# Kernel tuning notes

Hardware: AMD Instinct MI355X
Metric: run time of the kernel (lower is better)

Reference implementation:

```python
import jax, jax.numpy as jnp
import numpy as np

B, N_PER, DEG, F_IN, F_HID = 64, 1024, 16, 128, 128
E = B * N_PER * DEG  # 1,048,576 edges, grouped per graph


def setup_inputs() -> dict:
    key = jax.random.key(0)
    ks = jax.random.split(key, 16)
    n_total = B * N_PER
    x = jax.random.normal(ks[0], (n_total, F_IN), dtype=jnp.float32)
    # edges are random within each graph block
    local = jax.random.randint(ks[1], (2, E), 0, N_PER)
    offs = (jnp.arange(E, dtype=jnp.int64) // (N_PER * DEG)) * N_PER
    edge_index = (local.astype(jnp.int64) + offs[None, :])
    edge_weight = jax.random.uniform(ks[2], (E,), dtype=jnp.float32)
    batch_index = jnp.repeat(jnp.arange(B, dtype=jnp.int64), N_PER)
    s = 1.0 / np.sqrt(F_HID)
    params = {
        'W1': jax.random.normal(ks[3], (F_IN, F_HID)) * s,
        'b1': jnp.zeros((F_HID,), jnp.float32),
        'p1': jax.random.normal(ks[4], (F_HID,)) * s,
        'W2': jax.random.normal(ks[5], (F_HID, F_HID)) * s,
        'b2': jnp.zeros((F_HID,), jnp.float32),
        'p2': jax.random.normal(ks[6], (F_HID,)) * s,
        'W3': jax.random.normal(ks[7], (F_HID, F_HID)) * s,
        'b3': jnp.zeros((F_HID,), jnp.float32),
        'p3': jax.random.normal(ks[8], (F_HID,)) * s,
        'Wo': jax.random.normal(ks[9], (2 * F_HID, 1)) * s,
        'bo': jnp.zeros((1,), jnp.float32),
    }
    return {'x': x, 'edge_index': edge_index, 'edge_weight': edge_weight,
            'batch_index': batch_index, **params}


def _gcn_conv(x, src, dst, w, W, b):
    # GCNConv with add_self_loops=True, symmetric normalization, edge_weight.
    n = x.shape[0]
    xW = x @ W
    deg = jnp.zeros((n,), x.dtype).at[dst].add(w) + 1.0  # +1 from self-loop fill
    dinv = jax.lax.rsqrt(deg)
    norm = dinv[src] * w * dinv[dst]
    agg = jnp.zeros_like(xW).at[dst].add(norm[:, None] * xW[src])
    return agg + (dinv * dinv)[:, None] * xW + b  # self-loop term + bias


def _topk_pool(x, src, dst, w, p, n, k):
    # TopKPooling with nonlinearity=sigmoid, equal-size graphs (n -> k nodes).
    f = x.shape[1]
    xr = x.reshape(B, n, f)
    score = jax.nn.sigmoid((xr @ p) / jnp.linalg.norm(p))  # [B, n]
    vals, perm = jax.lax.top_k(score, k)                    # per-graph top-k
    xn = jnp.take_along_axis(xr, perm[:, :, None], axis=1) * vals[:, :, None]
    # inverse map old local idx -> new local idx (-1 if dropped)
    inv = jnp.full((B, n), -1, dtype=jnp.int32)
    inv = inv.at[jnp.arange(B)[:, None], perm].set(jnp.arange(k, dtype=jnp.int32)[None, :])
    g = src // n
    sl = inv[g, src % n]
    dl = inv[dst // n, dst % n]
    keep = (sl >= 0) & (dl >= 0)
    # dropped edges are masked to node 0 with weight 0 (contribute nothing)
    src2 = jnp.where(keep, g * k + sl, 0)
    dst2 = jnp.where(keep, (dst // n) * k + dl, 0)
    w2 = jnp.where(keep, w, jnp.zeros((), w.dtype))
    return xn.reshape(B * k, f), src2, dst2, w2


def reference(x, edge_index, edge_weight, batch_index,
              W1, b1, p1, W2, b2, p2, W3, b3, p3, Wo, bo):
    src, dst = edge_index[0], edge_index[1]
    w = edge_weight
    n = N_PER
    h = _gcn_conv(x, src, dst, w, W1, b1)
    h, src, dst, w = _topk_pool(h, src, dst, w, p1, n, n // 2); n //= 2
    h = jax.nn.relu(h)
    h = _gcn_conv(h, src, dst, w, W2, b2)
    h, src, dst, w = _topk_pool(h, src, dst, w, p2, n, n // 2); n //= 2
    h = jax.nn.relu(h)
    h = _gcn_conv(h, src, dst, w, W3, b3)
    h, src, dst, w = _topk_pool(h, src, dst, w, p3, n, n // 2); n //= 2
    h = jax.nn.relu(h)
    hr = h.reshape(B, n, -1)
    cat = jnp.concatenate([hr.max(axis=1), hr.mean(axis=1)], axis=1)  # gmp || gap
    out = jax.nn.sigmoid(cat @ Wo + bo)
    return out, cat
```

## Files before the change

kernel.cpp:

```cpp
#include <hip/hip_runtime.h>

#define NB 64
#define EDGES 1048576
#define NTOT  65536

struct __align__(8) CsrE { int s; float w; };

using bf16x8 = __attribute__((ext_vector_type(8))) short;
using f32x4  = __attribute__((ext_vector_type(4))) float;

__global__ void k_zerof(float* __restrict__ p, int n){
  int i=blockIdx.x*256+threadIdx.x; if(i<n) p[i]=0.f;
}

__device__ inline void split1(float x, unsigned &hi16, unsigned &lo16){
  unsigned b=__float_as_uint(x);
  unsigned h=(b+0x7FFFu+((b>>16)&1u))&0xFFFF0000u;
  float lf=x-__uint_as_float(h);
  unsigned lb=__float_as_uint(lf);
  hi16=h>>16;
  lo16=(lb+0x7FFFu+((lb>>16)&1u))>>16;
}

__device__ inline void split8(const float4&u, const float4&v, bf16x8&hi, bf16x8&lo){
  float e[8]={u.x,u.y,u.z,u.w,v.x,v.y,v.z,v.w};
  #pragma unroll
  for(int j=0;j<8;++j){
    unsigned h16,l16; split1(e[j],h16,l16);
    hi[j]=(short)h16; lo[j]=(short)l16;
  }
}

__global__ __launch_bounds__(256) void k_cntpack(const int* __restrict__ edst,
        const float* __restrict__ ew, int* __restrict__ chunkcnt, float* __restrict__ chunkw,
        const float* __restrict__ W1, const float* __restrict__ W2,
        const float* __restrict__ W3, unsigned* __restrict__ outp){
  __shared__ int lc[1024];
  __shared__ float lw[1024];
  int b=blockIdx.x, tid=threadIdx.x;
  if(b<512){
    int xcd=b&7, slot=b>>3;
    int graph=xcd*8+(slot&7), chunk=slot>>3;
    int e0=graph*16384+chunk*2048;
    for(int t=tid;t<1024;t+=256){ lc[t]=0; lw[t]=0.f; }
    __syncthreads();
    for(int e=e0+tid; e<e0+2048; e+=256){
      int dl=edst[e]&1023;
      atomicAdd(&lc[dl],1);
      atomicAdd(&lw[dl],ew[e]);
    }
    __syncthreads();
    for(int t=tid;t<1024;t+=256){
      chunkcnt[chunk*65536+graph*1024+t]=lc[t];
      chunkw  [chunk*65536+graph*1024+t]=lw[t];
    }
  } else {
    int wb=b-512, m=wb>>3;
    const float* W = (m==0)?W1:((m==1)?W2:W3);
    unsigned* o = outp + m*16384;
    for(int t=(wb&7)*256+tid; t<8192; t+=2048){
      int i=t&3, l=(t>>2)&63, c=(t>>8)&7, q=(t>>11)&3;
      int col=c*16+(l&15);
      int k0=q*32+((l>>4)<<3)+i*2;
      float x0=W[k0*128+col], x1=W[(k0+1)*128+col];
      unsigned h0,l0,h1,l1;
      split1(x0,h0,l0); split1(x1,h1,l1);
      int base=((q*8+c)*2)*256;
      o[base + l*4 + i]       = (h1<<16)|h0;
      o[base + 256 + l*4 + i] = (l1<<16)|l0;
    }
  }
}

template<bool G, int S>
__global__ __launch_bounds__(256) void mm_mfma(const float* __restrict__ X,
        const unsigned* __restrict__ Wpk, const int* __restrict__ selold,
        const float* __restrict__ score, float* __restrict__ Y, int gshift){
  __shared__ __align__(16) unsigned Wl[16384];
  const int RPB = 64*S;
  int b=blockIdx.x;
  int row0b;
  if(G){
    int xcd=b&7, slot=b>>3, bpg=1<<gshift;
    int graph=xcd*8+(slot>>gshift), idx=slot&(bpg-1);
    row0b = graph*(bpg*RPB) + idx*RPB;
  } else row0b = b*RPB;
  for(int t=threadIdx.x;t<4096;t+=256)
    ((uint4*)Wl)[t]=((const uint4*)Wpk)[t];
  const int wave=threadIdx.x>>6, lane=threadIdx.x&63;
  const int row0 = row0b + wave*(16*S);
  const int lrow=lane&15, lko=(lane>>4)<<3;
  int orow[S]; float scr[S];
  #pragma unroll
  for(int s=0;s<S;++s){
    int rr=row0+s*16+lrow;
    orow[s]=G?selold[rr]:rr;
    scr[s]=G?score[orow[s]]:1.f;
  }
  const f32x4 vzero={0.f,0.f,0.f,0.f};
  f32x4 acc[S][8];
  #pragma unroll
  for(int s=0;s<S;++s){
    #pragma unroll
    for(int c=0;c<8;++c) acc[s][c]=vzero;
  }
  __syncthreads();
  const char* wb=(const char*)Wl + lane*16;
  float4 u[S],v[S];
  #pragma unroll
  for(int s=0;s<S;++s){
    const float* xp=X+(size_t)orow[s]*128+lko;
    u[s]=*(const float4*)xp; v[s]=*(const float4*)(xp+4);
  }
  #pragma unroll
  for(int q=0;q<4;++q){
    float4 un[S],vn[S];
    if(q<3){
      #pragma unroll
      for(int s=0;s<S;++s){
        const float* xp=X+(size_t)orow[s]*128+(q+1)*32+lko;
        un[s]=*(const float4*)xp; vn[s]=*(const float4*)(xp+4);
      }
    }
    bf16x8 Ah[S],Al[S];
    #pragma unroll
    for(int s=0;s<S;++s){
      if(G){
        u[s].x=fmaxf(u[s].x*scr[s],0.f); u[s].y=fmaxf(u[s].y*scr[s],0.f);
        u[s].z=fmaxf(u[s].z*scr[s],0.f); u[s].w=fmaxf(u[s].w*scr[s],0.f);
        v[s].x=fmaxf(v[s].x*scr[s],0.f); v[s].y=fmaxf(v[s].y*scr[s],0.f);
        v[s].z=fmaxf(v[s].z*scr[s],0.f); v[s].w=fmaxf(v[s].w*scr[s],0.f);
      }
      split8(u[s],v[s],Ah[s],Al[s]);
    }
    #pragma unroll
    for(int c=0;c<8;++c){
      const bf16x8 bh=*(const bf16x8*)(wb + (q*8+c)*2048);
      const bf16x8 bl=*(const bf16x8*)(wb + (q*8+c)*2048 + 1024);
      #pragma unroll
      for(int s=0;s<S;++s){
        acc[s][c]=__builtin_amdgcn_mfma_f32_16x16x32_bf16(Ah[s],bh,acc[s][c],0,0,0);
        acc[s][c]=__builtin_amdgcn_mfma_f32_16x16x32_bf16(Al[s],bh,acc[s][c],0,0,0);
        acc[s][c]=__builtin_amdgcn_mfma_f32_16x16x32_bf16(Ah[s],bl,acc[s][c],0,0,0);
      }
    }
    if(q<3){
      #pragma unroll
      for(int s=0;s<S;++s){ u[s]=un[s]; v[s]=vn[s]; }
    }
  }
  const int dcol=lane&15, dr0=(lane>>4)<<2;
  #pragma unroll
  for(int s=0;s<S;++s){
    #pragma unroll
    for(int c=0;c<8;++c){
      #pragma unroll
      for(int r=0;r<4;++r){
        Y[(size_t)(row0+s*16+dr0+r)*128 + c*16 + dcol]=acc[s][c][r];
      }
    }
  }
}

__global__ __launch_bounds__(1024) void k_scatter2(const int* __restrict__ esrc,
        const int* __restrict__ edst, const float* __restrict__ ew,
        const int* __restrict__ chunkcnt, const float* __restrict__ chunkw,
        int* __restrict__ rowptr, float* __restrict__ dinv1, CsrE* __restrict__ csr){
  __shared__ int lc[1024];
  __shared__ int wsum[16];
  int b=blockIdx.x, i=threadIdx.x;
  int lane=i&63, w=i>>6;
  int xcd=b&7, slot=b>>3;
  int graph=xcd*8+(slot&7), chunk=slot>>3;
  int o=graph*1024+i;
  int ck[8];
  int c=0;
  #pragma unroll
  for(int k=0;k<8;++k){ ck[k]=chunkcnt[k*65536+o]; c+=ck[k]; }
  int v=c;
  #pragma unroll
  for(int off=1;off<64;off<<=1){ int t=__shfl_up(v,off,64); if(lane>=off) v+=t; }
  if(lane==63) wsum[w]=v;
  __syncthreads();
  int base=0;
  for(int k=0;k<w;++k) base+=wsum[k];
  int excl=base+v-c;
  int r0=graph*16384+excl;
  if(chunk==0){
    rowptr[o]=r0;
    float ws=0.f;
    #pragma unroll
    for(int k=0;k<8;++k) ws+=chunkw[k*65536+o];
    dinv1[o]=rsqrtf(ws+1.0f);
    if(graph==63 && i==1023) rowptr[65536]=EDGES;
  }
  int myfill=r0;
  for(int k=0;k<chunk;++k) myfill+=ck[k];
  lc[i]=myfill;
  __syncthreads();
  int e0=graph*16384+chunk*2048;
  for(int e=e0+i; e<e0+2048; e+=1024){
    int dl=edst[e]&1023;
    int pos=atomicAdd(&lc[dl],1);
    CsrE ce; ce.s=esrc[e]; ce.w=ew[e];
    csr[pos]=ce;
  }
}

template<bool F>
__global__ __launch_bounds__(256) void k_gather(const float* __restrict__ xw, const CsrE* __restrict__ csr,
        const int* __restrict__ rowptr, const int* __restrict__ map, const int* __restrict__ inv,
        const float* __restrict__ dinvv, const float* __restrict__ bias, const float* __restrict__ p,
        float* __restrict__ h, float* __restrict__ score, int gshift, int ns){
  int wv=threadIdx.x>>6, half=(threadIdx.x>>5)&1, hl=threadIdx.x&31;
  int b=blockIdx.x, xcd=b&7, slot=b>>3, bpg=1<<gshift;
  int graph=xcd*8+(slot>>gshift), idx=slot&(bpg-1);
  int v = graph*(bpg<<3) + (idx<<3) + wv*2 + half;
  if(v>=ns) return;
  int d0 = F? map[v] : v;
  float dv=dinvv[v];
  int rs=rowptr[d0], re=rowptr[d0+1];
  const int f4=hl*4;
  float4 accA={0.f,0.f,0.f,0.f}, accB={0.f,0.f,0.f,0.f};
  for(int base=rs; base<re; base+=32){
    int len=re-base; if(len>32) len=32;
    int sidx=0; float cf=0.f;
    if(hl<len){
      CsrE en=csr[base+hl];
      int s=en.s; bool live=true;
      if(F){ int t=inv[s]; live=(t>=0); s=live?t:0; }
      if(live){ sidx=s; cf=dinvv[s]*en.w; }
    }
    int len4=(len+3)&~3;
    for(int j=0;j<len4;j+=4){
      float c0=__shfl(cf,j,32),   c1=__shfl(cf,j+1,32);
      float c2=__shfl(cf,j+2,32), c3=__shfl(cf,j+3,32);
      int   s0=__shfl(sidx,j,32),   s1=__shfl(sidx,j+1,32);
      int   s2=__shfl(sidx,j+2,32), s3=__shfl(sidx,j+3,32);
      const float4 x0=*(const float4*)&xw[(size_t)s0*128+f4];
      const float4 x1=*(const float4*)&xw[(size_t)s1*128+f4];
      const float4 x2=*(const float4*)&xw[(size_t)s2*128+f4];
      const float4 x3=*(const float4*)&xw[(size_t)s3*128+f4];
      accA.x+=c0*x0.x; accA.y+=c0*x0.y; accA.z+=c0*x0.z; accA.w+=c0*x0.w;
      accB.x+=c1*x1.x; accB.y+=c1*x1.y; accB.z+=c1*x1.z; accB.w+=c1*x1.w;
      accA.x+=c2*x2.x; accA.y+=c2*x2.y; accA.z+=c2*x2.z; accA.w+=c2*x2.w;
      accB.x+=c3*x3.x; accB.y+=c3*x3.y; accB.z+=c3*x3.z; accB.w+=c3*x3.w;
    }
  }
  float4 acc; acc.x=accA.x+accB.x; acc.y=accA.y+accB.y;
  acc.z=accA.z+accB.z; acc.w=accA.w+accB.w;
  const float4 xv=*(const float4*)&xw[(size_t)v*128+f4];
  const float4 bv=*(const float4*)&bias[f4];
  float d2=dv*dv;
  float4 hv;
  hv.x=acc.x*dv + d2*xv.x + bv.x;
  hv.y=acc.y*dv + d2*xv.y + bv.y;
  hv.z=acc.z*dv + d2*xv.z + bv.z;
  hv.w=acc.w*dv + d2*xv.w + bv.w;
  *(float4*)&h[(size_t)v*128+f4]=hv;
  const float4 pv=*(const float4*)&p[f4];
  float z=hv.x*pv.x+hv.y*pv.y+hv.z*pv.z+hv.w*pv.w;
  float pp=pv.x*pv.x+pv.y*pv.y+pv.z*pv.z+pv.w*pv.w;
  #pragma unroll
  for(int m=16;m>0;m>>=1){ z+=__shfl_xor(z,m,32); pp+=__shfl_xor(pp,m,32); }
  if(hl==0) score[v]=1.0f/(1.0f+expf(-z/sqrtf(pp)));
}

template<int N, int K, int MODE>
__global__ __launch_bounds__(N) void k_topk(const float* __restrict__ score,
        int* __restrict__ inv, int* __restrict__ selold,
        const int* __restrict__ inv1s, const int* __restrict__ sel1s,
        int* __restrict__ inv12, int* __restrict__ map12,
        const int* __restrict__ rowptr, const CsrE* __restrict__ csr,
        float* __restrict__ dinv_out,
        const float* __restrict__ h3, const float* __restrict__ Wo,
        const float* __restrict__ bo, float* __restrict__ outp){
  __shared__ unsigned hist[256];
  __shared__ int wsum[16];
  __shared__ int c_sh, r_sh;
  __shared__ float red[128];
  int g=blockIdx.x, i=threadIdx.x;
  int lane=i&63, w=i>>6;
  int gv=g*N+i;
  unsigned key=__float_as_uint(score[gv]);
  int st=1;
  int R=K;
  #pragma unroll
  for(int pass=0; pass<4; ++pass){
    int shift=24-pass*8;
    if(i<256) hist[i]=0;
    __syncthreads();
    unsigned byte=(key>>shift)&255u;
    if(st==1) atomicAdd(&hist[byte],1u);
    __syncthreads();
    unsigned hcnt=0, sfx=0;
    if(i<256){
      hcnt=hist[i]; sfx=hcnt;
      #pragma unroll
      for(int off=1;off<64;off<<=1){
        unsigned t=__shfl_down(sfx,off,64);
        if(lane+off<64) sfx+=t;
      }
      if(lane==0) wsum[w]=(int)sfx;
    }
    __syncthreads();
    if(i<256){
      int tot=0;
      for(int k=w+1;k<4;++k) tot+=wsum[k];
      int Si=(int)sfx+tot;
      int A=Si-(int)hcnt;
      if(A<R && R<=Si){ c_sh=i; r_sh=R-A; }
    }
    __syncthreads();
    int c=c_sh; R=r_sh;
    if(st==1){
      if((int)byte>c) st=2;
      else if((int)byte<c) st=0;
    }
    __syncthreads();
  }
  int alive=(st==1)?1:0;
  unsigned long long mA=__ballot(alive);
  int rA=__popcll(mA & ((1ULL<<lane)-1ULL));
  if(lane==0) wsum[w]=__popcll(mA);
  __syncthreads();
  int offA=0;
  for(int k=0;k<w;++k) offA+=wsum[k];
  int tie_rank=offA+rA;
  int sel=(st==2)||(st==1 && tie_rank<R);
  __syncthreads();
  unsigned long long mS=__ballot(sel);
  int rS=__popcll(mS & ((1ULL<<lane)-1ULL));
  if(lane==0) wsum[w]=__popcll(mS);
  __syncthreads();
  int offS=0;
  for(int k=0;k<w;++k) offS+=wsum[k];
  int ng=g*K+offS+rS;
  if(sel && ng<NB*K){ inv[gv]=ng; selold[ng]=gv; }
  else inv[gv]=-1;
  if(MODE==1){
    __syncthreads();
    for(int t=i; t<K; t+=N){
      int v=g*K+t;
      int d0=selold[v];
      int rs=rowptr[d0], re=rowptr[d0+1];
      float s0=0.f,s1=0.f,s2=0.f,s3=0.f;
      int e=rs;
      for(; e+4<=re; e+=4){
        CsrE e0=csr[e], e1=csr[e+1], e2=csr[e+2], e3=csr[e+3];
        if(inv[e0.s]>=0) s0+=e0.w;
        if(inv[e1.s]>=0) s1+=e1.w;
        if(inv[e2.s]>=0) s2+=e2.w;
        if(inv[e3.s]>=0) s3+=e3.w;
      }
      for(; e<re; ++e){
        CsrE en=csr[e];
        if(inv[en.s]>=0) s0+=en.w;
      }
      dinv_out[v]=rsqrtf((s0+s1)+(s2+s3)+1.0f);
    }
  }
  if(MODE==2){
    __syncthreads();
    for(int t=i; t<1024; t+=N){
      int v0=g*1024+t;
      int q=inv1s[v0];
      inv12[v0]=(q>=0)?inv[q]:-1;
    }
    for(int t=i; t<K; t+=N){
      int v=g*K+t;
      map12[v]=sel1s[selold[v]];
    }
    __syncthreads();
    for(int t=i; t<K; t+=N){
      int v=g*K+t;
      int d0=map12[v];
      int rs=rowptr[d0], re=rowptr[d0+1];
      float s0=0.f,s1=0.f,s2=0.f,s3=0.f;
      int e=rs;
      for(; e+4<=re; e+=4){
        CsrE e0=csr[e], e1=csr[e+1], e2=csr[e+2], e3=csr[e+3];
        if(inv12[e0.s]>=0) s0+=e0.w;
        if(inv12[e1.s]>=0) s1+=e1.w;
        if(inv12[e2.s]>=0) s2+=e2.w;
        if(inv12[e3.s]>=0) s3+=e3.w;
      }
      for(; e<re; ++e){
        CsrE en=csr[e];
        if(inv12[en.s]>=0) s0+=en.w;
      }
      dinv_out[v]=rsqrtf((s0+s1)+(s2+s3)+1.0f);
    }
  }
  if(MODE==3){
    __syncthreads();
    int f=i;
    float mx=-3.4e38f, sm=0.f;
    if(f<128){
      for(int nd=0;nd<128;++nd){
        int old=selold[g*128+nd];
        float vv=fmaxf(h3[(size_t)old*128+f]*score[old],0.f);
        mx=fmaxf(mx,vv); sm+=vv;
      }
      float mean=sm*(1.0f/128.0f);
      outp[64+g*256+f]    =mx;
      outp[64+g*256+128+f]=mean;
      red[f]=mx*Wo[f]+mean*Wo[128+f];
    }
    __syncthreads();
    for(int off=64;off>0;off>>=1){
      if(f<off) red[f]+=red[f+off];
      __syncthreads();
    }
    if(f==0){ float z=red[0]+bo[0]; outp[g]=1.0f/(1.0f+expf(-z)); }
  }
}

extern "C" void kernel_launch(void* const* d_in, const int* in_sizes, int n_in,
                              void* d_out, int out_size, void* d_ws, size_t ws_size,
                              hipStream_t stream) {
  (void)in_sizes; (void)n_in;
  const float* x  = (const float*)d_in[0];
  const int*   ei = (const int*)d_in[1];
  const float* ew = (const float*)d_in[2];
  const float* W1=(const float*)d_in[4];  const float* b1=(const float*)d_in[5];  const float* p1=(const float*)d_in[6];
  const float* W2=(const float*)d_in[7];  const float* b2=(const float*)d_in[8];  const float* p2=(const float*)d_in[9];
  const float* W3=(const float*)d_in[10]; const float* b3=(const float*)d_in[11]; const float* p3=(const float*)d_in[12];
  const float* Wo=(const float*)d_in[13]; const float* bo=(const float*)d_in[14];
  float* out=(float*)d_out;

  char* ws=(char*)d_ws;
  size_t cur=0;
  float* slot0=(float*)(ws+cur); cur+=33554432;
  float* slot1=(float*)(ws+cur); cur+=33554432;
  CsrE*  csr  =(CsrE*)(ws+cur);  cur+=(size_t)EDGES*8;
  int*   chunkcnt=(int*)(ws+cur); cur+=2097152;
  float* chunkw  =(float*)(ws+cur); cur+=2097152;
  int*   rowptr=(int*) (ws+cur); cur+=262400;
  float* dinv1=(float*)(ws+cur); cur+=262144;
  float* dinv2=(float*)(ws+cur); cur+=131072;
  float* dinv3=(float*)(ws+cur); cur+=65536;
  float* sc1  =(float*)(ws+cur); cur+=262144;
  float* sc2  =(float*)(ws+cur); cur+=131072;
  float* sc3  =(float*)(ws+cur); cur+=65536;
  int*   inv1 =(int*)  (ws+cur); cur+=262144;
  int*   inv2 =(int*)  (ws+cur); cur+=131072;
  int*   invS =(int*)  (ws+cur); cur+=65536;
  int*   inv12=(int*)  (ws+cur); cur+=262144;
  int*   sel1 =(int*)  (ws+cur); cur+=131072;
  int*   sel2 =(int*)  (ws+cur); cur+=65536;
  int*   sel3 =(int*)  (ws+cur); cur+=32768;
  int*   map12=(int*)  (ws+cur); cur+=65536;
  unsigned* wpk=(unsigned*)(ws+cur); cur+=196608;

  if (ws_size < cur) {
    k_zerof<<<(out_size+255)/256,256,0,stream>>>(out,out_size);
    return;
  }

  const int* esrc=ei; const int* edst=ei+EDGES;

  k_cntpack<<<536,256,0,stream>>>(edst,ew,chunkcnt,chunkw,W1,W2,W3,wpk);
  mm_mfma<false,2><<<NTOT/128,256,0,stream>>>(x,wpk,nullptr,nullptr,slot0,0);
  k_scatter2<<<512,1024,0,stream>>>(esrc,edst,ew,chunkcnt,chunkw,rowptr,dinv1,csr);
  k_gather<false><<<NTOT/8,256,0,stream>>>(slot0,csr,rowptr,nullptr,nullptr,
                                           dinv1,b1,p1,slot1,sc1,7,NTOT);
  k_topk<1024,512,1><<<NB,1024,0,stream>>>(sc1,inv1,sel1,nullptr,nullptr,nullptr,nullptr,
                                           rowptr,csr,dinv2,nullptr,nullptr,nullptr,nullptr);

  mm_mfma<true,1><<<32768/64,256,0,stream>>>(slot1,wpk+16384,sel1,sc1,slot0,3);
  k_gather<true><<<32768/8,256,0,stream>>>(slot0,csr,rowptr,sel1,inv1,
                                           dinv2,b2,p2,slot1,sc2,6,32768);
  k_topk<512,256,2><<<NB,512,0,stream>>>(sc2,inv2,sel2,inv1,sel1,inv12,map12,
                                         rowptr,csr,dinv3,nullptr,nullptr,nullptr,nullptr);

  mm_mfma<true,1><<<16384/64,256,0,stream>>>(slot1,wpk+32768,sel2,sc2,slot0,2);
  k_gather<true><<<16384/8,256,0,stream>>>(slot0,csr,rowptr,map12,inv12,
                                           dinv3,b3,p3,slot1,sc3,5,16384);
  k_topk<256,128,3><<<NB,256,0,stream>>>(sc3,invS,sel3,nullptr,nullptr,nullptr,nullptr,
                                         nullptr,nullptr,nullptr,slot1,Wo,bo,out);
}
```

Before: 270.4 us.

## Move post-topk degree recomputation into extra blocks of the following matmul kernel

The pooled-graph degree/dinv computation (and the inv12/map12 remapping) previously ran inside the top-k kernel, using only 64 blocks with long serial per-thread loops. It now runs as extra blocks appended to the next mm_mfma launch, so it is spread across more blocks and overlaps with the matmul work. The risk is load imbalance among the mixed blocks. A mode-3 block also depends on inv12 values written by other threads of the same block, which relies on the __syncthreads placement within that block being correct.

```diff
diff --git a/kernel.cpp b/kernel.cpp
--- a/kernel.cpp
+++ b/kernel.cpp
@@ -72,93 +72,147 @@
   }
 }
 
-template<bool G, int S>
+template<bool G, int S, int EPI, int MMB>
 __global__ __launch_bounds__(256) void mm_mfma(const float* __restrict__ X,
         const unsigned* __restrict__ Wpk, const int* __restrict__ selold,
-        const float* __restrict__ score, float* __restrict__ Y, int gshift){
+        const float* __restrict__ score, float* __restrict__ Y, int gshift,
+        const int* __restrict__ inv1, const int* __restrict__ sel1,
+        const int* __restrict__ inv2, const int* __restrict__ sel2,
+        int* __restrict__ inv12, int* __restrict__ map12,
+        const int* __restrict__ rowptr, const CsrE* __restrict__ csr,
+        float* __restrict__ dinv_out){
   __shared__ __align__(16) unsigned Wl[16384];
-  const int RPB = 64*S;
   int b=blockIdx.x;
-  int row0b;
-  if(G){
-    int xcd=b&7, slot=b>>3, bpg=1<<gshift;
-    int graph=xcd*8+(slot>>gshift), idx=slot&(bpg-1);
-    row0b = graph*(bpg*RPB) + idx*RPB;
-  } else row0b = b*RPB;
-  for(int t=threadIdx.x;t<4096;t+=256)
-    ((uint4*)Wl)[t]=((const uint4*)Wpk)[t];
-  const int wave=threadIdx.x>>6, lane=threadIdx.x&63;
-  const int row0 = row0b + wave*(16*S);
-  const int lrow=lane&15, lko=(lane>>4)<<3;
-  int orow[S]; float scr[S];
-  #pragma unroll
-  for(int s=0;s<S;++s){
-    int rr=row0+s*16+lrow;
-    orow[s]=G?selold[rr]:rr;
-    scr[s]=G?score[orow[s]]:1.f;
-  }
-  const f32x4 vzero={0.f,0.f,0.f,0.f};
-  f32x4 acc[S][8];
-  #pragma unroll
-  for(int s=0;s<S;++s){
-    #pragma unroll
-    for(int c=0;c<8;++c) acc[s][c]=vzero;
-  }
-  __syncthreads();
-  const char* wb=(const char*)Wl + lane*16;
-  float4 u[S],v[S];
-  #pragma unroll
-  for(int s=0;s<S;++s){
-    const float* xp=X+(size_t)orow[s]*128+lko;
-    u[s]=*(const float4*)xp; v[s]=*(const float4*)(xp+4);
-  }
-  #pragma unroll
-  for(int q=0;q<4;++q){
-    float4 un[S],vn[S];
-    if(q<3){
+  if(b<MMB){
+    const int RPB = 64*S;
+    int row0b;
+    if(G){
+      int xcd=b&7, slot=b>>3, bpg=1<<gshift;
+      int graph=xcd*8+(slot>>gshift), idx=slot&(bpg-1);
+      row0b = graph*(bpg*RPB) + idx*RPB;
+    } else row0b = b*RPB;
+    for(int t=threadIdx.x;t<4096;t+=256)
+      ((uint4*)Wl)[t]=((const uint4*)Wpk)[t];
+    const int wave=threadIdx.x>>6, lane=threadIdx.x&63;
+    const int row0 = row0b + wave*(16*S);
+    const int lrow=lane&15, lko=(lane>>4)<<3;
+    int orow[S]; float scr[S];
+    #pragma unroll
+    for(int s=0;s<S;++s){
+      int rr=row0+s*16+lrow;
+      orow[s]=G?selold[rr]:rr;
+      scr[s]=G?score[orow[s]]:1.f;
+    }
+    const f32x4 vzero={0.f,0.f,0.f,0.f};
+    f32x4 acc[S][8];
+    #pragma unroll
+    for(int s=0;s<S;++s){
+      #pragma unroll
+      for(int c=0;c<8;++c) acc[s][c]=vzero;
+    }
+    __syncthreads();
+    const char* wb=(const char*)Wl + lane*16;
+    float4 u[S],v[S];
+    #pragma unroll
+    for(int s=0;s<S;++s){
+      const float* xp=X+(size_t)orow[s]*128+lko;
+      u[s]=*(const float4*)xp; v[s]=*(const float4*)(xp+4);
+    }
+    #pragma unroll
+    for(int q=0;q<4;++q){
+      float4 un[S],vn[S];
+      if(q<3){
+        #pragma unroll
+        for(int s=0;s<S;++s){
+          const float* xp=X+(size_t)orow[s]*128+(q+1)*32+lko;
+          un[s]=*(const float4*)xp; vn[s]=*(const float4*)(xp+4);
+        }
+      }
+      bf16x8 Ah[S],Al[S];
       #pragma unroll
       for(int s=0;s<S;++s){
-        const float* xp=X+(size_t)orow[s]*128+(q+1)*32+lko;
-        un[s]=*(const float4*)xp; vn[s]=*(const float4*)(xp+4);
-      }
-    }
-    bf16x8 Ah[S],Al[S];
+        if(G){
+          u[s].x=fmaxf(u[s].x*scr[s],0.f); u[s].y=fmaxf(u[s].y*scr[s],0.f);
+          u[s].z=fmaxf(u[s].z*scr[s],0.f); u[s].w=fmaxf(u[s].w*scr[s],0.f);
+          v[s].x=fmaxf(v[s].x*scr[s],0.f); v[s].y=fmaxf(v[s].y*scr[s],0.f);
+          v[s].z=fmaxf(v[s].z*scr[s],0.f); v[s].w=fmaxf(v[s].w*scr[s],0.f);
+        }
+        split8(u[s],v[s],Ah[s],Al[s]);
+      }
+      #pragma unroll
+      for(int c=0;c<8;++c){
+        const bf16x8 bh=*(const bf16x8*)(wb + (q*8+c)*2048);
+        const bf16x8 bl=*(const bf16x8*)(wb + (q*8+c)*2048 + 1024);
+        #pragma unroll
+        for(int s=0;s<S;++s){
+          acc[s][c]=__builtin_amdgcn_mfma_f32_16x16x32_bf16(Ah[s],bh,acc[s][c],0,0,0);
+          acc[s][c]=__builtin_amdgcn_mfma_f32_16x16x32_bf16(Al[s],bh,acc[s][c],0,0,0);
+          acc[s][c]=__builtin_amdgcn_mfma_f32_16x16x32_bf16(Ah[s],bl,acc[s][c],0,0,0);
+        }
+      }
+      if(q<3){
+        #pragma unroll
+        for(int s=0;s<S;++s){ u[s]=un[s]; v[s]=vn[s]; }
+      }
+    }
+    const int dcol=lane&15, dr0=(lane>>4)<<2;
     #pragma unroll
     for(int s=0;s<S;++s){
-      if(G){
-        u[s].x=fmaxf(u[s].x*scr[s],0.f); u[s].y=fmaxf(u[s].y*scr[s],0.f);
-        u[s].z=fmaxf(u[s].z*scr[s],0.f); u[s].w=fmaxf(u[s].w*scr[s],0.f);
-        v[s].x=fmaxf(v[s].x*scr[s],0.f); v[s].y=fmaxf(v[s].y*scr[s],0.f);
-        v[s].z=fmaxf(v[s].z*scr[s],0.f); v[s].w=fmaxf(v[s].w*scr[s],0.f);
-      }
-      split8(u[s],v[s],Ah[s],Al[s]);
-    }
-    #pragma unroll
-    for(int c=0;c<8;++c){
-      const bf16x8 bh=*(const bf16x8*)(wb + (q*8+c)*2048);
-      const bf16x8 bl=*(const bf16x8*)(wb + (q*8+c)*2048 + 1024);
       #pragma unroll
-      for(int s=0;s<S;++s){
-        acc[s][c]=__builtin_amdgcn_mfma_f32_16x16x32_bf16(Ah[s],bh,acc[s][c],0,0,0);
-        acc[s][c]=__builtin_amdgcn_mfma_f32_16x16x32_bf16(Al[s],bh,acc[s][c],0,0,0);
-        acc[s][c]=__builtin_amdgcn_mfma_f32_16x16x32_bf16(Ah[s],bl,acc[s][c],0,0,0);
-      }
-    }
-    if(q<3){
-      #pragma unroll
-      for(int s=0;s<S;++s){ u[s]=un[s]; v[s]=vn[s]; }
-    }
-  }
-  const int dcol=lane&15, dr0=(lane>>4)<<2;
-  #pragma unroll
-  for(int s=0;s<S;++s){
-    #pragma unroll
-    for(int c=0;c<8;++c){
-      #pragma unroll
-      for(int r=0;r<4;++r){
-        Y[(size_t)(row0+s*16+dr0+r)*128 + c*16 + dcol]=acc[s][c][r];
-      }
-    }
+      for(int c=0;c<8;++c){
+        #pragma unroll
+        for(int r=0;r<4;++r){
+          Y[(size_t)(row0+s*16+dr0+r)*128 + c*16 + dcol]=acc[s][c][r];
+        }
+      }
+    }
+    return;
+  }
+  if(EPI==2){
+    int v=(b-MMB)*256+threadIdx.x;
+    int d0=sel1[v];
+    int rs=rowptr[d0], re=rowptr[d0+1];
+    float s0=0.f,s1=0.f,s2=0.f,s3=0.f;
+    int e=rs;
+    for(; e+4<=re; e+=4){
+      CsrE e0=csr[e], e1=csr[e+1], e2=csr[e+2], e3=csr[e+3];
+      if(inv1[e0.s]>=0) s0+=e0.w;
+      if(inv1[e1.s]>=0) s1+=e1.w;
+      if(inv1[e2.s]>=0) s2+=e2.w;
+      if(inv1[e3.s]>=0) s3+=e3.w;
+    }
+    for(; e<re; ++e){
+      CsrE en=csr[e];
+      if(inv1[en.s]>=0) s0+=en.w;
+    }
+    dinv_out[v]=rsqrtf((s0+s1)+(s2+s3)+1.0f);
+  }
+  if(EPI==3){
+    int g=b-MMB, i=threadIdx.x;
+    for(int t=i; t<1024; t+=256){
+      int v0=g*1024+t;
+      int q=inv1[v0];
+      inv12[v0]=(q>=0)?inv2[q]:-1;
+    }
+    int v=g*256+i;
+    map12[v]=sel1[sel2[v]];
+    __syncthreads();
+    int d0=map12[v];
+    int rs=rowptr[d0], re=rowptr[d0+1];
+    float s0=0.f,s1=0.f,s2=0.f,s3=0.f;
+    int e=rs;
+    for(; e+4<=re; e+=4){
+      CsrE e0=csr[e], e1=csr[e+1], e2=csr[e+2], e3=csr[e+3];
+      if(inv12[e0.s]>=0) s0+=e0.w;
+      if(inv12[e1.s]>=0) s1+=e1.w;
+      if(inv12[e2.s]>=0) s2+=e2.w;
+      if(inv12[e3.s]>=0) s3+=e3.w;
+    }
+    for(; e<re; ++e){
+      CsrE en=csr[e];
+      if(inv12[en.s]>=0) s0+=en.w;
+    }
+    dinv_out[v]=rsqrtf((s0+s1)+(s2+s3)+1.0f);
   }
 }
 
@@ -269,10 +323,6 @@
 template<int N, int K, int MODE>
 __global__ __launch_bounds__(N) void k_topk(const float* __restrict__ score,
         int* __restrict__ inv, int* __restrict__ selold,
-        const int* __restrict__ inv1s, const int* __restrict__ sel1s,
-        int* __restrict__ inv12, int* __restrict__ map12,
-        const int* __restrict__ rowptr, const CsrE* __restrict__ csr,
-        float* __restrict__ dinv_out,
         const float* __restrict__ h3, const float* __restrict__ Wo,
         const float* __restrict__ bo, float* __restrict__ outp){
   __shared__ unsigned hist[256];
@@ -338,60 +388,6 @@
   int ng=g*K+offS+rS;
   if(sel && ng<NB*K){ inv[gv]=ng; selold[ng]=gv; }
   else inv[gv]=-1;
-  if(MODE==1){
-    __syncthreads();
-    for(int t=i; t<K; t+=N){
-      int v=g*K+t;
-      int d0=selold[v];
-      int rs=rowptr[d0], re=rowptr[d0+1];
-      float s0=0.f,s1=0.f,s2=0.f,s3=0.f;
-      int e=rs;
-      for(; e+4<=re; e+=4){
-        CsrE e0=csr[e], e1=csr[e+1], e2=csr[e+2], e3=csr[e+3];
-        if(inv[e0.s]>=0) s0+=e0.w;
-        if(inv[e1.s]>=0) s1+=e1.w;
-        if(inv[e2.s]>=0) s2+=e2.w;
-        if(inv[e3.s]>=0) s3+=e3.w;
-      }
-      for(; e<re; ++e){
-        CsrE en=csr[e];
-        if(inv[en.s]>=0) s0+=en.w;
-      }
-      dinv_out[v]=rsqrtf((s0+s1)+(s2+s3)+1.0f);
-    }
-  }
-  if(MODE==2){
-    __syncthreads();
-    for(int t=i; t<1024; t+=N){
-      int v0=g*1024+t;
-      int q=inv1s[v0];
-      inv12[v0]=(q>=0)?inv[q]:-1;
-    }
-    for(int t=i; t<K; t+=N){
-      int v=g*K+t;
-      map12[v]=sel1s[selold[v]];
-    }
-    __syncthreads();
-    for(int t=i; t<K; t+=N){
-      int v=g*K+t;
-      int d0=map12[v];
-      int rs=rowptr[d0], re=rowptr[d0+1];
-      float s0=0.f,s1=0.f,s2=0.f,s3=0.f;
-      int e=rs;
-      for(; e+4<=re; e+=4){
-        CsrE e0=csr[e], e1=csr[e+1], e2=csr[e+2], e3=csr[e+3];
-        if(inv12[e0.s]>=0) s0+=e0.w;
-        if(inv12[e1.s]>=0) s1+=e1.w;
-        if(inv12[e2.s]>=0) s2+=e2.w;
-        if(inv12[e3.s]>=0) s3+=e3.w;
-      }
-      for(; e<re; ++e){
-        CsrE en=csr[e];
-        if(inv12[en.s]>=0) s0+=en.w;
-      }
-      dinv_out[v]=rsqrtf((s0+s1)+(s2+s3)+1.0f);
-    }
-  }
   if(MODE==3){
     __syncthreads();
     int f=i;
@@ -461,22 +457,22 @@
   const int* esrc=ei; const int* edst=ei+EDGES;
 
   k_cntpack<<<536,256,0,stream>>>(edst,ew,chunkcnt,chunkw,W1,W2,W3,wpk);
-  mm_mfma<false,2><<<NTOT/128,256,0,stream>>>(x,wpk,nullptr,nullptr,slot0,0);
+  mm_mfma<false,2,0,512><<<512,256,0,stream>>>(x,wpk,nullptr,nullptr,slot0,0,
+      nullptr,nullptr,nullptr,nullptr,nullptr,nullptr,nullptr,nullptr,nullptr);
   k_scatter2<<<512,1024,0,stream>>>(esrc,edst,ew,chunkcnt,chunkw,rowptr,dinv1,csr);
   k_gather<false><<<NTOT/8,256,0,stream>>>(slot0,csr,rowptr,nullptr,nullptr,
                                            dinv1,b1,p1,slot1,sc1,7,NTOT);
-  k_topk<1024,512,1><<<NB,1024,0,stream>>>(sc1,inv1,sel1,nullptr,nullptr,nullptr,nullptr,
-                                           rowptr,csr,dinv2,nullptr,nullptr,nullptr,nullptr);
-
-  mm_mfma<true,1><<<32768/64,256,0,stream>>>(slot1,wpk+16384,sel1,sc1,slot0,3);
+  k_topk<1024,512,0><<<NB,1024,0,stream>>>(sc1,inv1,sel1,nullptr,nullptr,nullptr,nullptr);
+
+  mm_mfma<true,1,2,512><<<640,256,0,stream>>>(slot1,wpk+16384,sel1,sc1,slot0,3,
+      inv1,sel1,nullptr,nullptr,nullptr,nullptr,rowptr,csr,dinv2);
   k_gather<true><<<32768/8,256,0,stream>>>(slot0,csr,rowptr,sel1,inv1,
                                            dinv2,b2,p2,slot1,sc2,6,32768);
-  k_topk<512,256,2><<<NB,512,0,stream>>>(sc2,inv2,sel2,inv1,sel1,inv12,map12,
-                                         rowptr,csr,dinv3,nullptr,nullptr,nullptr,nullptr);
-
-  mm_mfma<true,1><<<16384/64,256,0,stream>>>(slot1,wpk+32768,sel2,sc2,slot0,2);
+  k_topk<512,256,0><<<NB,512,0,stream>>>(sc2,inv2,sel2,nullptr,nullptr,nullptr,nullptr);
+
+  mm_mfma<true,1,3,256><<<320,256,0,stream>>>(slot1,wpk+32768,sel2,sc2,slot0,2,
+      inv1,sel1,inv2,sel2,inv12,map12,rowptr,csr,dinv3);
   k_gather<true><<<16384/8,256,0,stream>>>(slot0,csr,rowptr,map12,inv12,
                                            dinv3,b3,p3,slot1,sc3,5,16384);
-  k_topk<256,128,3><<<NB,256,0,stream>>>(sc3,invS,sel3,nullptr,nullptr,nullptr,nullptr,
-                                         nullptr,nullptr,nullptr,slot1,Wo,bo,out);
-}
+  k_topk<256,128,3><<<NB,256,0,stream>>>(sc3,invS,sel3,slot1,Wo,bo,out);
+}
```

Result: faster. 263.5 us (-2.6%).
